# Kernel tuning notes

Hardware: AMD Instinct MI355X
Metric: run time of the kernel (lower is better)

Reference implementation:

```python
import jax, jax.numpy as jnp
import numpy as np

K = 12          # number of agents (== max_other_agents, required by blowup)
MOA = 12        # max_other_agents
H, W, D = 24, 24, 8
C0, C1, C2, C3 = 32, 16, 16, 8
PHYS, MENT, ACT = 16, 16, 16
HSZ = C3 * H * W                      # 4608
INP = HSZ + PHYS + MENT + MOA * PHYS + MOA * MENT  # 5024
EPS = 1e-5
MIX = 0.9


def setup_inputs() -> dict:
    key = jax.random.key(0)
    ks = jax.random.split(key, 32)
    s = 0.02
    d = {
        "x": jax.random.normal(ks[0], (K, C0, D, H, W), jnp.float32),
        "p": jax.random.normal(ks[1], (K, PHYS), jnp.float32),
        "m": jax.random.normal(ks[2], (K, MENT), jnp.float32),
        "vis": jax.random.uniform(ks[3], (K, MOA), jnp.float32),
        "conv1_w": jax.random.normal(ks[4], (C1, C0, D), jnp.float32) * s,
        "conv1_b": jnp.zeros((C1,), jnp.float32),
        "bn1_g": jnp.ones((C1,), jnp.float32),
        "bn1_b": jnp.zeros((C1,), jnp.float32),
        "conv2_w": jax.random.normal(ks[5], (C2, C1, 3, 3), jnp.float32) * s,
        "conv2_b": jnp.zeros((C2,), jnp.float32),
        "bn2_g": jnp.ones((C2,), jnp.float32),
        "bn2_b": jnp.zeros((C2,), jnp.float32),
        "conv3_w": jax.random.normal(ks[6], (C3, C2, 5, 5), jnp.float32) * s,
        "conv3_b": jnp.zeros((C3,), jnp.float32),
        "bn3_g": jnp.ones((C3,), jnp.float32),
        "bn3_b": jnp.zeros((C3,), jnp.float32),
        "phys_w": jax.random.normal(ks[7], (PHYS, PHYS), jnp.float32) * s,
        "phys_b": jnp.zeros((PHYS,), jnp.float32),
        "ment_w": jax.random.normal(ks[8], (MENT, MENT), jnp.float32) * s,
        "ment_b": jnp.zeros((MENT,), jnp.float32),
        "w_ih": jax.random.normal(ks[9], (4 * HSZ, INP), jnp.float32) * s,
        "w_hh": jax.random.normal(ks[10], (4 * HSZ, HSZ), jnp.float32) * s,
        "b_ih": jnp.zeros((4 * HSZ,), jnp.float32),
        "b_hh": jnp.zeros((4 * HSZ,), jnp.float32),
        "ah_w": jax.random.normal(ks[11], (128, HSZ), jnp.float32) * s,
        "ah_b": jnp.zeros((128,), jnp.float32),
        "act_w": jax.random.normal(ks[12], (ACT, 128), jnp.float32) * s,
        "act_b": jnp.zeros((ACT,), jnp.float32),
        "inf_w": jax.random.normal(ks[13], (MOA * MENT, HSZ), jnp.float32) * s,
        "inf_b": jnp.zeros((MOA * MENT,), jnp.float32),
    }
    return d


def _bn2d(x, g, b):
    # batch-norm in training mode (batch statistics, biased var), x: [N,C,H,W]
    mu = jnp.mean(x, axis=(0, 2, 3), keepdims=True)
    var = jnp.mean((x - mu) ** 2, axis=(0, 2, 3), keepdims=True)
    return (x - mu) * jax.lax.rsqrt(var + EPS) * g[None, :, None, None] + b[None, :, None, None]


def _conv2d(x, w, b):
    y = jax.lax.conv_general_dilated(x, w, (1, 1), 'SAME',
                                     dimension_numbers=('NCHW', 'OIHW', 'NCHW'))
    return y + b[None, :, None, None]


def reference(x, p, m, vis,
              conv1_w, conv1_b, bn1_g, bn1_b,
              conv2_w, conv2_b, bn2_g, bn2_b,
              conv3_w, conv3_b, bn3_g, bn3_b,
              phys_w, phys_b, ment_w, ment_b,
              w_ih, w_hh, b_ih, b_hh,
              ah_w, ah_b, act_w, act_b, inf_w, inf_b):
    k = K
    # Conv3d with kernel (D,1,1) == contraction over channel and depth dims
    h1 = jnp.einsum('bcdhw,ocd->bohw', x, conv1_w) + conv1_b[None, :, None, None]
    h1 = jax.nn.relu(_bn2d(h1, bn1_g, bn1_b))          # [k,C1,H,W]
    h2 = jax.nn.relu(_bn2d(_conv2d(h1, conv2_w, conv2_b), bn2_g, bn2_b))
    h3 = jax.nn.relu(_bn2d(_conv2d(h2, conv3_w, conv3_b), bn3_g, bn3_b))  # [k,C3,H,W]

    ag = jnp.concatenate([jax.nn.relu(p @ phys_w.T + phys_b),
                          jax.nn.relu(m @ ment_w.T + ment_b)], axis=1)     # [k,PHYS+MENT]

    # blowup: broadcasted outer product (k == MOA so padding is a no-op)
    other_p = jax.nn.relu(p @ phys_w.T + phys_b)                           # [MOA,PHYS]
    phys_inp = vis[:, :, None] * other_p[None, :, :]                       # [k,MOA,PHYS]

    # mixed mental reps (old_ment is None on first step)
    other_m = MIX * jnp.broadcast_to(m[None, :, :], (k, MOA, MENT))
    ment_inp = jax.nn.relu(other_m.reshape(k * MOA, MENT) @ ment_w.T + ment_b)

    lstm_in = jnp.concatenate([h3.reshape(k, -1), ag,
                               phys_inp.reshape(k, -1),
                               ment_inp.reshape(k, -1)], axis=1)           # [k,INP]

    # single LSTM step with zero initial state (torch gate order i,f,g,o)
    gates = lstm_in @ w_ih.T + b_ih + b_hh                                 # h0 = 0
    i_g, f_g, g_g, o_g = jnp.split(gates, 4, axis=1)
    c = jax.nn.sigmoid(i_g) * jnp.tanh(g_g)                                # c0 = 0
    h = jax.nn.sigmoid(o_g) * jnp.tanh(c)                                  # [k,HSZ]

    hr = jax.nn.relu(h)
    old_ment = (hr @ inf_w.T + inf_b).reshape(k, MOA, MENT)
    act = jax.nn.relu(hr @ ah_w.T + ah_b) @ act_w.T + act_b               # [k,ACT]
    return act, old_ment
```

## Files before the change

kernel.cpp:

```cpp
#include <hip/hip_runtime.h>
#include <hip/hip_bf16.h>
#include <stdint.h>

typedef __hip_bfloat16 bf16;
typedef __attribute__((ext_vector_type(8))) short short8;
typedef __attribute__((ext_vector_type(4))) float floatx4;
typedef __attribute__((ext_vector_type(4))) float float4v;

#define DEV static __device__ __forceinline__

DEV float b2f(bf16 x) { return __bfloat162float(x); }
DEV float sb2f(short s) { return __uint_as_float(((unsigned int)(unsigned short)s) << 16); }
DEV short f2s(float f) { union { bf16 h; short s; } u; u.h = __float2bfloat16(f); return u.s; }
DEV float ld(const void* base, size_t idx, int f32) {
  return f32 ? ((const float*)base)[idx] : b2f(((const bf16*)base)[idx]);
}


static const size_t OFF_T1   = 0;
static const size_t OFF_T2   = 442368;
static const size_t OFF_T3   = 884736;
static const size_t OFF_BN1  = 1105920;
static const size_t OFF_BN2  = 1106048;
static const size_t OFF_BN3  = 1106176;
static const size_t OFF_PO   = 1106240;
static const size_t OFF_MA   = 1107008;
static const size_t OFF_MM   = 1107776;
static const size_t OFF_LSTM = 1108544;
static const size_t OFF_GATE = 1269312;
static const size_t OFF_HR   = 2154048;
static const size_t OFF_AH   = 2264640;
static const size_t OFF_BAR  = 2270784;

#define GRID 216

union SmemU {
  struct { float wl[4][256]; } c1;
  struct { float hin[16 * 676]; float wl[4 * 144]; } c2;
  struct { float hin[16 * 784]; float wl[2 * 400]; } c3;
  short8 A[2560];
};

#define GSYNC()                                                                   \
  do {                                                                            \
    __syncthreads();                                                              \
    ++bar_round;                                                                  \
    if (tid == 0) {                                                               \
      __threadfence();                                                            \
      atomicAdd(bar, 1);                                                          \
      int tgt = bar_round * GRID;                                                 \
      int sp = 0;                                                                 \
      while (__hip_atomic_load(bar, __ATOMIC_RELAXED,                             \
                               __HIP_MEMORY_SCOPE_AGENT) < tgt) {                 \
        __builtin_amdgcn_s_sleep(1);                                              \
        if (++sp > 100000000) break;        \
      }                                                                           \
      __threadfence();                                                            \
    }                                                                             \
    __syncthreads();                                                              \
  } while (0)

DEV void bn_block(const float* __restrict__ src, const void* __restrict__ g,
                  const void* __restrict__ bb, float* __restrict__ prm,
                  int C, int c, int f32, float* ls, float* ls2, int tid) {
  float s = 0.f, s2 = 0.f;
  for (int i = tid; i < 12 * 576; i += 256) {
    int b = i / 576, pq = i % 576;
    float v = src[((size_t)b * C + c) * 576 + pq];
    s += v; s2 += v * v;
  }
#pragma unroll
  for (int o = 1; o < 64; o <<= 1) { s += __shfl_xor(s, o, 64); s2 += __shfl_xor(s2, o, 64); }
  int wv = tid >> 6;
  if ((tid & 63) == 0) { ls[wv] = s; ls2[wv] = s2; }
  __syncthreads();
  if (tid == 0) {
    float S = ls[0] + ls[1] + ls[2] + ls[3];
    float S2 = ls2[0] + ls2[1] + ls2[2] + ls2[3];
    float mean = S * (1.f / 6912.f);
    float var = S2 * (1.f / 6912.f) - mean * mean;
    float sc = ld(g, c, f32) * rsqrtf(var + 1e-5f);
    prm[c * 2] = sc;
    prm[c * 2 + 1] = ld(bb, c, f32) - mean * sc;
  }
}

__global__ __launch_bounds__(256, 2) void k_all(
    const void* __restrict__ x, const void* __restrict__ p,
    const void* __restrict__ m, const void* __restrict__ vis,
    const void* __restrict__ c1w, const void* __restrict__ c1b,
    const void* __restrict__ g1, const void* __restrict__ b1,
    const void* __restrict__ c2w, const void* __restrict__ c2b,
    const void* __restrict__ g2, const void* __restrict__ b2,
    const void* __restrict__ c3w, const void* __restrict__ c3b,
    const void* __restrict__ g3, const void* __restrict__ b3,
    const void* __restrict__ pw, const void* __restrict__ pb,
    const void* __restrict__ mw, const void* __restrict__ mb,
    const void* __restrict__ w_ih, const void* __restrict__ b_ih,
    const void* __restrict__ b_hh,
    const void* __restrict__ ah_w, const void* __restrict__ ah_b,
    const void* __restrict__ act_w, const void* __restrict__ act_b,
    const void* __restrict__ inf_w, const void* __restrict__ inf_b,
    float* __restrict__ t1, float* __restrict__ t2, float* __restrict__ t3,
    float* __restrict__ bn1p, float* __restrict__ bn2p, float* __restrict__ bn3p,
    float* __restrict__ phys_out, float* __restrict__ ment_ag, float* __restrict__ mmv,
    bf16* __restrict__ lstm_pad, float* __restrict__ gates, bf16* __restrict__ hr,
    float* __restrict__ ah_ws, void* __restrict__ out, int* bar) {
  __shared__ SmemU smem;
  __shared__ float bnls[4], bnls2[4];
  const int bid = blockIdx.x, tid = threadIdx.x;
  const int f32 = (((const unsigned int*)g1)[0] == 0x3F800000u) ? 1 : 0;
  int bar_round = 0;

  if (bid < 48) {
    int b = bid >> 2, og = bid & 3;
    for (int i = tid; i < 1024; i += 256) {
      int ol = i >> 8, cd = i & 255;
      smem.c1.wl[ol][cd] = ld(c1w, (size_t)(og * 4 + ol) * 256 + cd, f32);
    }
    __syncthreads();
    if (tid < 192) {
      float acc[3][4];
#pragma unroll
      for (int pp = 0; pp < 3; ++pp)
#pragma unroll
        for (int o = 0; o < 4; ++o) acc[pp][o] = ld(c1b, og * 4 + o, f32);
      size_t xb = (size_t)b * 256 * 576;
      for (int cd = 0; cd < 256; ++cd) {
        float x0 = ld(x, xb + cd * 576 + tid, f32);
        float x1 = ld(x, xb + cd * 576 + tid + 192, f32);
        float x2 = ld(x, xb + cd * 576 + tid + 384, f32);
#pragma unroll
        for (int o = 0; o < 4; ++o) {
          float wv = smem.c1.wl[o][cd];
          acc[0][o] += x0 * wv; acc[1][o] += x1 * wv; acc[2][o] += x2 * wv;
        }
      }
#pragma unroll
      for (int pp = 0; pp < 3; ++pp)
#pragma unroll
        for (int o = 0; o < 4; ++o)
          t1[((size_t)b * 16 + og * 4 + o) * 576 + tid + pp * 192] = acc[pp][o];
    }
  }
  GSYNC();

  if (bid < 16) bn_block(t1, g1, b1, bn1p, 16, bid, f32, bnls, bnls2, tid);
  GSYNC();

  if (bid < 48) {
    int b = bid >> 2, og = bid & 3;
    float* hin = smem.c2.hin;
    float* wl2 = smem.c2.wl;
    for (int i = tid; i < 16 * 676; i += 256) hin[i] = 0.f;
    for (int i = tid; i < 576; i += 256) wl2[i] = ld(c2w, (size_t)og * 576 + i, f32);
    __syncthreads();
    for (int i = tid; i < 16 * 576; i += 256) {
      int c = i / 576, pq = i % 576, h = pq / 24, wq = pq % 24;
      float v = t1[((size_t)b * 16 + c) * 576 + pq];
      v = v * bn1p[c * 2] + bn1p[c * 2 + 1];
      hin[c * 676 + (h + 1) * 26 + (wq + 1)] = fmaxf(v, 0.f);
    }
    __syncthreads();
    for (int it = tid; it < 4 * 576; it += 256) {
      int ol = it / 576, pq = it % 576, h = pq / 24, wq = pq % 24;
      float acc = ld(c2b, og * 4 + ol, f32);
#pragma unroll
      for (int c = 0; c < 16; ++c) {
        const float* hp = &hin[c * 676 + h * 26 + wq];
        const float* wp2 = &wl2[ol * 144 + c * 9];
#pragma unroll
        for (int ky = 0; ky < 3; ++ky)
#pragma unroll
          for (int kx = 0; kx < 3; ++kx)
            acc += hp[ky * 26 + kx] * wp2[ky * 3 + kx];
      }
      t2[((size_t)b * 16 + og * 4 + ol) * 576 + pq] = acc;
    }
  }
  GSYNC();

  if (bid < 16) bn_block(t2, g2, b2, bn2p, 16, bid, f32, bnls, bnls2, tid);
  GSYNC();

  if (bid < 48) {
    int b = bid >> 2, og = bid & 3;
    float* hin = smem.c3.hin;
    float* wl3 = smem.c3.wl;
    for (int i = tid; i < 16 * 784; i += 256) hin[i] = 0.f;
    for (int i = tid; i < 800; i += 256) wl3[i] = ld(c3w, (size_t)og * 800 + i, f32);
    __syncthreads();
    for (int i = tid; i < 16 * 576; i += 256) {
      int c = i / 576, pq = i % 576, h = pq / 24, wq = pq % 24;
      float v = t2[((size_t)b * 16 + c) * 576 + pq];
      v = v * bn2p[c * 2] + bn2p[c * 2 + 1];
      hin[c * 784 + (h + 2) * 28 + (wq + 2)] = fmaxf(v, 0.f);
    }
    __syncthreads();
    for (int it = tid; it < 2 * 576; it += 256) {
      int ol = it / 576, pq = it % 576, h = pq / 24, wq = pq % 24;
      float acc = ld(c3b, og * 2 + ol, f32);
#pragma unroll
      for (int c = 0; c < 16; ++c) {
        const float* hp = &hin[c * 784 + h * 28 + wq];
        const float* wp3 = &wl3[ol * 400 + c * 25];
#pragma unroll
        for (int ky = 0; ky < 5; ++ky)
#pragma unroll
          for (int kx = 0; kx < 5; ++kx)
            acc += hp[ky * 28 + kx] * wp3[ky * 5 + kx];
      }
      t3[((size_t)b * 8 + og * 2 + ol) * 576 + pq] = acc;
    }
  }
  GSYNC();

  if (bid < 8) {
    bn_block(t3, g3, b3, bn3p, 8, bid, f32, bnls, bnls2, tid);
  } else if (bid == 8 && tid < 192) {
    int j = tid >> 4, o = tid & 15;
    float a1 = ld(pb, o, f32), a2 = ld(mb, o, f32), a3 = ld(mb, o, f32);
#pragma unroll
    for (int i = 0; i < 16; ++i) {
      a1 += ld(p, j * 16 + i, f32) * ld(pw, o * 16 + i, f32);
      float mvv = ld(m, j * 16 + i, f32);
      float wvv = ld(mw, o * 16 + i, f32);
      a2 += mvv * wvv;
      a3 += 0.9f * mvv * wvv;
    }
    phys_out[tid] = fmaxf(a1, 0.f);
    ment_ag[tid] = fmaxf(a2, 0.f);
    mmv[tid] = fmaxf(a3, 0.f);
  }
  GSYNC();

  for (int idx = bid * 256 + tid; idx < 80384; idx += GRID * 256) {
    int mrow = idx / 5024, k = idx % 5024;
    float v = 0.f;
    if (mrow < 12) {
      if (k < 4608) {
        int c = k / 576, pos = k % 576;
        float t = t3[((size_t)mrow * 8 + c) * 576 + pos];
        v = fmaxf(t * bn3p[c * 2] + bn3p[c * 2 + 1], 0.f);
      } else if (k < 4624) {
        v = phys_out[mrow * 16 + (k - 4608)];
      } else if (k < 4640) {
        v = ment_ag[mrow * 16 + (k - 4624)];
      } else if (k < 4832) {
        int r = k - 4640;
        v = ld(vis, mrow * 12 + (r >> 4), f32) * phys_out[r];
      } else {
        v = mmv[k - 4832];
      }
    }
    lstm_pad[idx] = __float2bfloat16(v);
  }
  GSYNC();

  {
    int wv = tid >> 6, lane = tid & 63;
    int jb0 = bid * 64;
    int jr0 = (jb0 < 4608) ? jb0 : jb0 + 4608;
    int jl = jr0 + wv * 16 + (lane & 15);
    int quad = lane >> 4;
    floatx4 acc = {0.f, 0.f, 0.f, 0.f};
    const short* lp = (const short*)lstm_pad;
    const short* wp_base = (const short*)w_ih + (size_t)jl * 5024 + quad * 8;
    const float* wf_base = (const float*)w_ih + (size_t)jl * 5024 + quad * 8;
#pragma unroll 1
    for (int ph = 0; ph < 4; ++ph) {
      int kbase = ph * 1280;
      int KB = (ph < 3) ? 40 : 37;
      int nch = KB * 64;
      for (int c = tid; c < nch; c += 256) {
        int kb = c >> 6, r = c & 63, mr = r & 15, qc = (r >> 4) & 3;
        int k = kbase + kb * 32 + qc * 8;
        smem.A[c] = *(const short8*)(lp + (size_t)mr * 5024 + k);
      }
      __syncthreads();
      if (!f32) {
        const short* wp = wp_base + kbase;
        for (int kb = 0; kb < KB; ++kb) {
          short8 av = smem.A[kb * 64 + lane];
          short8 bv = *(const short8*)(wp + kb * 32);
          acc = __builtin_amdgcn_mfma_f32_16x16x32_bf16(av, bv, acc, 0, 0, 0);
        }
      } else {
        const float* wpf = wf_base + kbase;
        for (int kb = 0; kb < KB; ++kb) {
          short8 av = smem.A[kb * 64 + lane];
          float4v w0 = *(const float4v*)(wpf + kb * 32);
          float4v w1 = *(const float4v*)(wpf + kb * 32 + 4);
          short8 bv;
          bv[0] = f2s(w0[0]); bv[1] = f2s(w0[1]); bv[2] = f2s(w0[2]); bv[3] = f2s(w0[3]);
          bv[4] = f2s(w1[0]); bv[5] = f2s(w1[1]); bv[6] = f2s(w1[2]); bv[7] = f2s(w1[3]);
          acc = __builtin_amdgcn_mfma_f32_16x16x32_bf16(av, bv, acc, 0, 0, 0);
        }
      }
      __syncthreads();
    }
    float bsum = ld(b_ih, jl, f32) + ld(b_hh, jl, f32);
#pragma unroll
    for (int q = 0; q < 4; ++q) {
      int mrow2 = quad * 4 + q;
      if (mrow2 < 12) gates[(size_t)mrow2 * 18432 + jl] = acc[q] + bsum;
    }
  }
  GSYNC();

  {
    int idx = bid * 256 + tid;
    int mrow = idx / 4608, h = idx % 4608;
    const float* gm = gates + (size_t)mrow * 18432;
    float ig = gm[h], gg = gm[9216 + h], og2 = gm[13824 + h];
    float c = (1.f / (1.f + __expf(-ig))) * tanhf(gg);
    float hv = (1.f / (1.f + __expf(-og2))) * tanhf(c);
    hr[idx] = __float2bfloat16(fmaxf(hv, 0.f));
  }
  GSYNC();

  if (bid < 80) {
    int gw = bid * 4 + (tid >> 6);
    int lane = tid & 63;
    size_t wrow = (gw < 192) ? ((size_t)gw * 4608) : ((size_t)(gw - 192) * 4608);
    const void* wbase = (gw < 192) ? inf_w : ah_w;
    float acc[12];
#pragma unroll
    for (int q = 0; q < 12; ++q) acc[q] = 0.f;
    const short* hp = (const short*)hr;
    for (int it = 0; it < 9; ++it) {
      int k = it * 512 + lane * 8;
      float wf[8];
      if (f32) {
        const float* wrf = (const float*)wbase + wrow + k;
        float4v a0 = *(const float4v*)(wrf);
        float4v a1 = *(const float4v*)(wrf + 4);
        wf[0] = a0[0]; wf[1] = a0[1]; wf[2] = a0[2]; wf[3] = a0[3];
        wf[4] = a1[0]; wf[5] = a1[1]; wf[6] = a1[2]; wf[7] = a1[3];
      } else {
        short8 wv8 = *(const short8*)((const short*)wbase + wrow + k);
#pragma unroll
        for (int e = 0; e < 8; ++e) wf[e] = sb2f(wv8[e]);
      }
#pragma unroll
      for (int q = 0; q < 12; ++q) {
        short8 hv8 = *(const short8*)(hp + q * 4608 + k);
#pragma unroll
        for (int e = 0; e < 8; ++e)
          acc[q] += sb2f(hv8[e]) * wf[e];
      }
    }
#pragma unroll
    for (int s = 1; s < 64; s <<= 1)
#pragma unroll
      for (int q = 0; q < 12; ++q) acc[q] += __shfl_xor(acc[q], s, 64);
    float v = acc[0];
#pragma unroll
    for (int q = 1; q < 12; ++q)
      if (lane == q) v = acc[q];
    if (lane < 12) {
      if (gw < 192) {
        float v2 = v + ld(inf_b, gw, f32);
        size_t oi = 192 + (size_t)lane * 192 + gw;
        if (f32) ((float*)out)[oi] = v2;
        else ((bf16*)out)[oi] = __float2bfloat16(v2);
      } else {
        int a = gw - 192;
        ah_ws[lane * 128 + a] = fmaxf(v + ld(ah_b, a, f32), 0.f);
      }
    }
  }
  GSYNC();

  if (bid == 0 && tid < 192) {
    int mrow = tid >> 4, a = tid & 15;
    float acc = ld(act_b, a, f32);
    for (int c = 0; c < 128; ++c)
      acc += ah_ws[mrow * 128 + c] * ld(act_w, a * 128 + c, f32);
    if (f32) ((float*)out)[tid] = acc;
    else ((bf16*)out)[tid] = __float2bfloat16(acc);
  }
}

extern "C" void kernel_launch(void* const* d_in, const int* in_sizes, int n_in,
                              void* d_out, int out_size, void* d_ws, size_t ws_size,
                              hipStream_t stream) {
  const void* x       = d_in[0];
  const void* p       = d_in[1];
  const void* m       = d_in[2];
  const void* vis     = d_in[3];
  const void* conv1_w = d_in[4];
  const void* conv1_b = d_in[5];
  const void* bn1_g   = d_in[6];
  const void* bn1_b   = d_in[7];
  const void* conv2_w = d_in[8];
  const void* conv2_b = d_in[9];
  const void* bn2_g   = d_in[10];
  const void* bn2_b   = d_in[11];
  const void* conv3_w = d_in[12];
  const void* conv3_b = d_in[13];
  const void* bn3_g   = d_in[14];
  const void* bn3_b   = d_in[15];
  const void* phys_w  = d_in[16];
  const void* phys_b  = d_in[17];
  const void* ment_w  = d_in[18];
  const void* ment_b  = d_in[19];
  const void* w_ih    = d_in[20];
  const void* b_ih    = d_in[22];
  const void* b_hh    = d_in[23];
  const void* ah_w    = d_in[24];
  const void* ah_b    = d_in[25];
  const void* act_w   = d_in[26];
  const void* act_b   = d_in[27];
  const void* inf_w   = d_in[28];
  const void* inf_b   = d_in[29];

  char* ws = (char*)d_ws;
  float* t1       = (float*)(ws + OFF_T1);
  float* t2       = (float*)(ws + OFF_T2);
  float* t3       = (float*)(ws + OFF_T3);
  float* bn1p     = (float*)(ws + OFF_BN1);
  float* bn2p     = (float*)(ws + OFF_BN2);
  float* bn3p     = (float*)(ws + OFF_BN3);
  float* phys_out = (float*)(ws + OFF_PO);
  float* ment_ag  = (float*)(ws + OFF_MA);
  float* mmv      = (float*)(ws + OFF_MM);
  bf16* lstm_pad  = (bf16*)(ws + OFF_LSTM);
  float* gates    = (float*)(ws + OFF_GATE);
  bf16* hr        = (bf16*)(ws + OFF_HR);
  float* ah_ws    = (float*)(ws + OFF_AH);
  int*  bar       = (int*)(ws + OFF_BAR);

  hipMemsetAsync(bar, 0, 8, stream);
  k_all<<<dim3(GRID), dim3(256), 0, stream>>>(
      x, p, m, vis, conv1_w, conv1_b, bn1_g, bn1_b,
      conv2_w, conv2_b, bn2_g, bn2_b, conv3_w, conv3_b, bn3_g, bn3_b,
      phys_w, phys_b, ment_w, ment_b, w_ih, b_ih, b_hh,
      ah_w, ah_b, act_w, act_b, inf_w, inf_b,
      t1, t2, t3, bn1p, bn2p, bn3p, phys_out, ment_ag, mmv,
      lstm_pad, gates, hr, ah_ws, d_out, bar);
}
```

Measured before the change: 980.8 us.

## Replace MFMA LSTM input GEMM with per-wave FMA dot products over weight rows

The LSTM input-gate GEMM no longer stages the activation matrix into shared memory and runs bf16 MFMA tiles. Each wave now handles 8 weight rows per pass, reads weights and the 12 activation rows directly from global memory, accumulates 96 fp32 sums in scalar FMA, and finishes with a butterfly shuffle reduction. The goal is to stream the weight matrix from memory with wide per-lane loads and fewer block-wide syncs. In exchange it uses far more registers (hence launch bounds lowered to 1 block per SU), does much more ALU work, and adds a long shuffle reduction.

Result: no change. 978.9 us (-0.2%).

```diff
diff --git a/kernel.cpp b/kernel.cpp
--- a/kernel.cpp
+++ b/kernel.cpp
@@ -4,14 +4,13 @@
 
 typedef __hip_bfloat16 bf16;
 typedef __attribute__((ext_vector_type(8))) short short8;
-typedef __attribute__((ext_vector_type(4))) float floatx4;
+typedef __attribute__((ext_vector_type(4))) short s4v;
 typedef __attribute__((ext_vector_type(4))) float float4v;
 
 #define DEV static __device__ __forceinline__
 
 DEV float b2f(bf16 x) { return __bfloat162float(x); }
 DEV float sb2f(short s) { return __uint_as_float(((unsigned int)(unsigned short)s) << 16); }
-DEV short f2s(float f) { union { bf16 h; short s; } u; u.h = __float2bfloat16(f); return u.s; }
 DEV float ld(const void* base, size_t idx, int f32) {
   return f32 ? ((const float*)base)[idx] : b2f(((const bf16*)base)[idx]);
 }
@@ -38,7 +37,6 @@
   struct { float wl[4][256]; } c1;
   struct { float hin[16 * 676]; float wl[4 * 144]; } c2;
   struct { float hin[16 * 784]; float wl[2 * 400]; } c3;
-  short8 A[2560];
 };
 
 #define GSYNC()                                                                   \
@@ -85,7 +83,7 @@
   }
 }
 
-__global__ __launch_bounds__(256, 2) void k_all(
+__global__ __launch_bounds__(256, 1) void k_all(
     const void* __restrict__ x, const void* __restrict__ p,
     const void* __restrict__ m, const void* __restrict__ vis,
     const void* __restrict__ c1w, const void* __restrict__ c1b,
@@ -259,51 +257,84 @@
 
   {
     int wv = tid >> 6, lane = tid & 63;
-    int jb0 = bid * 64;
-    int jr0 = (jb0 < 4608) ? jb0 : jb0 + 4608;
-    int jl = jr0 + wv * 16 + (lane & 15);
-    int quad = lane >> 4;
-    floatx4 acc = {0.f, 0.f, 0.f, 0.f};
+    int wid = bid * 4 + wv;
     const short* lp = (const short*)lstm_pad;
-    const short* wp_base = (const short*)w_ih + (size_t)jl * 5024 + quad * 8;
-    const float* wf_base = (const float*)w_ih + (size_t)jl * 5024 + quad * 8;
 #pragma unroll 1
-    for (int ph = 0; ph < 4; ++ph) {
-      int kbase = ph * 1280;
-      int KB = (ph < 3) ? 40 : 37;
-      int nch = KB * 64;
-      for (int c = tid; c < nch; c += 256) {
-        int kb = c >> 6, r = c & 63, mr = r & 15, qc = (r >> 4) & 3;
-        int k = kbase + kb * 32 + qc * 8;
-        smem.A[c] = *(const short8*)(lp + (size_t)mr * 5024 + k);
-      }
-      __syncthreads();
+    for (int pass = 0; pass < 2; ++pass) {
+      int grp = wid * 2 + pass;
+      int vj0 = grp * 8;
+      int j0 = (vj0 < 4608) ? vj0 : vj0 + 4608;
+      float acc[12][8];
+#pragma unroll
+      for (int q = 0; q < 12; ++q)
+#pragma unroll
+        for (int r = 0; r < 8; ++r) acc[q][r] = 0.f;
       if (!f32) {
-        const short* wp = wp_base + kbase;
-        for (int kb = 0; kb < KB; ++kb) {
-          short8 av = smem.A[kb * 64 + lane];
-          short8 bv = *(const short8*)(wp + kb * 32);
-          acc = __builtin_amdgcn_mfma_f32_16x16x32_bf16(av, bv, acc, 0, 0, 0);
+        const short* wb = (const short*)w_ih + (size_t)j0 * 5024;
+#pragma unroll 1
+        for (int it = 0; it < 20; ++it) {
+          int kb = it * 256 + lane * 4;
+          if (kb < 5024) {
+            float wr[8][4];
+#pragma unroll
+            for (int r = 0; r < 8; ++r) {
+              s4v w4 = *(const s4v*)(wb + (size_t)r * 5024 + kb);
+              wr[r][0] = sb2f(w4[0]); wr[r][1] = sb2f(w4[1]);
+              wr[r][2] = sb2f(w4[2]); wr[r][3] = sb2f(w4[3]);
+            }
+#pragma unroll
+            for (int q = 0; q < 12; ++q) {
+              s4v l4 = *(const s4v*)(lp + q * 5024 + kb);
+              float l0 = sb2f(l4[0]), l1 = sb2f(l4[1]);
+              float l2 = sb2f(l4[2]), l3 = sb2f(l4[3]);
+#pragma unroll
+              for (int r = 0; r < 8; ++r)
+                acc[q][r] += l0 * wr[r][0] + l1 * wr[r][1] + l2 * wr[r][2] + l3 * wr[r][3];
+            }
+          }
         }
       } else {
-        const float* wpf = wf_base + kbase;
-        for (int kb = 0; kb < KB; ++kb) {
-          short8 av = smem.A[kb * 64 + lane];
-          float4v w0 = *(const float4v*)(wpf + kb * 32);
-          float4v w1 = *(const float4v*)(wpf + kb * 32 + 4);
-          short8 bv;
-          bv[0] = f2s(w0[0]); bv[1] = f2s(w0[1]); bv[2] = f2s(w0[2]); bv[3] = f2s(w0[3]);
-          bv[4] = f2s(w1[0]); bv[5] = f2s(w1[1]); bv[6] = f2s(w1[2]); bv[7] = f2s(w1[3]);
-          acc = __builtin_amdgcn_mfma_f32_16x16x32_bf16(av, bv, acc, 0, 0, 0);
+        const float* wbf = (const float*)w_ih + (size_t)j0 * 5024;
+#pragma unroll 1
+        for (int it = 0; it < 20; ++it) {
+          int kb = it * 256 + lane * 4;
+          if (kb < 5024) {
+            float wr[8][4];
+#pragma unroll
+            for (int r = 0; r < 8; ++r) {
+              float4v w4 = *(const float4v*)(wbf + (size_t)r * 5024 + kb);
+              wr[r][0] = w4[0]; wr[r][1] = w4[1]; wr[r][2] = w4[2]; wr[r][3] = w4[3];
+            }
+#pragma unroll
+            for (int q = 0; q < 12; ++q) {
+              s4v l4 = *(const s4v*)(lp + q * 5024 + kb);
+              float l0 = sb2f(l4[0]), l1 = sb2f(l4[1]);
+              float l2 = sb2f(l4[2]), l3 = sb2f(l4[3]);
+#pragma unroll
+              for (int r = 0; r < 8; ++r)
+                acc[q][r] += l0 * wr[r][0] + l1 * wr[r][1] + l2 * wr[r][2] + l3 * wr[r][3];
+            }
+          }
         }
       }
-      __syncthreads();
-    }
-    float bsum = ld(b_ih, jl, f32) + ld(b_hh, jl, f32);
-#pragma unroll
-    for (int q = 0; q < 4; ++q) {
-      int mrow2 = quad * 4 + q;
-      if (mrow2 < 12) gates[(size_t)mrow2 * 18432 + jl] = acc[q] + bsum;
+#pragma unroll
+      for (int s = 1; s < 64; s <<= 1)
+#pragma unroll
+        for (int q = 0; q < 12; ++q)
+#pragma unroll
+          for (int r = 0; r < 8; ++r)
+            acc[q][r] += __shfl_xor(acc[q][r], s, 64);
+#pragma unroll
+      for (int r = 0; r < 8; ++r) {
+        float v = acc[0][r];
+#pragma unroll
+        for (int q = 1; q < 12; ++q)
+          if (lane == q) v = acc[q][r];
+        if (lane < 12) {
+          int j = j0 + r;
+          gates[(size_t)lane * 18432 + j] = v + ld(b_ih, j, f32) + ld(b_hh, j, f32);
+        }
+      }
     }
   }
   GSYNC();
@@ -431,7 +462,7 @@
   float* ah_ws    = (float*)(ws + OFF_AH);
   int*  bar       = (int*)(ws + OFF_BAR);
 
-  hipMemsetAsync(bar, 0, 8, stream);
+  (void)hipMemsetAsync(bar, 0, 8, stream);
   k_all<<<dim3(GRID), dim3(256), 0, stream>>>(
       x, p, m, vis, conv1_w, conv1_b, bn1_g, bn1_b,
       conv2_w, conv2_b, bn2_g, bn2_b, conv3_w, conv3_b, bn3_g, bn3_b,
```
